# Optimization experiments

Measured on AMD Instinct MI355X. Metric: run time of the kernel, lower is better.

Reference implementation:

```python
import jax, jax.numpy as jnp
import numpy as np

DIM_HEAD = 64
LN_EPS = 1e-6  # flax nn.LayerNorm default


def setup_inputs() -> dict:
    key = jax.random.key(0)
    ks = jax.random.split(key, 5)
    B, N, D, H, Dh = 4, 1024, 768, 12, 64
    x = jax.random.normal(ks[0], (B, N, D), dtype=jnp.float32)
    Wq = jax.random.normal(ks[1], (D, H, Dh), dtype=jnp.float32) * (1.0 / np.sqrt(D))
    Wk = jax.random.normal(ks[2], (D, H, Dh), dtype=jnp.float32) * (1.0 / np.sqrt(D))
    Wv = jax.random.normal(ks[3], (D, H, Dh), dtype=jnp.float32) * (1.0 / np.sqrt(D))
    theta = jax.random.normal(ks[4], (H, H), dtype=jnp.float32) * (1.0 / np.sqrt(H))
    ln_scale = jnp.ones((N,), dtype=jnp.float32)
    ln_bias = jnp.zeros((N,), dtype=jnp.float32)
    return {"x": x, "Wq": Wq, "Wk": Wk, "Wv": Wv, "theta": theta,
            "ln_scale": ln_scale, "ln_bias": ln_bias}


def reference(x, Wq, Wk, Wv, theta, ln_scale, ln_bias):
    # x: [B, N, D]; W*: [D, H, Dh]; theta: [H, H]; ln_*: [N]
    q = jnp.einsum('bnd,dhe->bnhe', x, Wq) / jnp.sqrt(jnp.float32(DIM_HEAD))
    k = jnp.einsum('bnd,dhe->bnhe', x, Wk)
    v = jnp.einsum('bnd,dhe->bnhe', x, Wv)
    # attention scores over key axis: [B, H, N, N]
    attn = jnp.einsum('bqhd,bkhd->bhqk', q, k)
    attn = jax.nn.softmax(attn, axis=-1)
    # cross-head theta mixing: 'h i, b h q k -> b i q k'
    attn = jnp.einsum('hi,bhqk->biqk', theta, attn)
    # LayerNorm over last (key) axis with learnable scale/bias of shape [N]
    mean = jnp.mean(attn, axis=-1, keepdims=True)
    var = jnp.mean(jnp.square(attn - mean), axis=-1, keepdims=True)
    attn = (attn - mean) * jax.lax.rsqrt(var + LN_EPS) * ln_scale + ln_bias
    # note: output indexed by k (as in the original source einsum)
    out = jnp.einsum('bhqk,bqhd->bkhd', attn, v)
    B, N, H, Dh = out.shape
    return out.reshape(B, N, H * Dh)
```

## Files before the change

### kernel.cpp

```cpp
#include <hip/hip_runtime.h>

#define NB    4
#define NSEQ  1024
#define DMODEL 768
#define NH    12
#define DH    64

typedef __bf16 bf16x8 __attribute__((ext_vector_type(8)));
typedef __bf16 bf16x4 __attribute__((ext_vector_type(4)));
typedef float  floatx4 __attribute__((ext_vector_type(4)));
typedef unsigned int u32;

static __device__ __forceinline__ float bf2f(unsigned short u) {
    return __uint_as_float(((unsigned)u) << 16);
}
static __device__ __forceinline__ unsigned short f2bf(float f) {
    unsigned u = __float_as_uint(f);
    u += 0x7FFFu + ((u >> 16) & 1u);
    return (unsigned short)(u >> 16);
}
static __device__ __forceinline__ unsigned short f2bf_hw(float f) {
    __bf16 b = (__bf16)f;
    return *(unsigned short*)&b;
}

static __device__ __forceinline__ void gl_lds16(const void* g, void* l) {
    __builtin_amdgcn_global_load_lds(
        (const __attribute__((address_space(1))) unsigned int*)g,
        (__attribute__((address_space(3))) unsigned int*)l, 16, 0, 0);
}

__global__ __launch_bounds__(256) void cast_x(
    const float* __restrict__ x, unsigned short* __restrict__ xb)
{
    const int g = blockIdx.x * 256 + threadIdx.x;
    const size_t base = (size_t)g * 8;
    float4 a = *(const float4*)(x + base);
    float4 b = *(const float4*)(x + base + 4);
    unsigned short o[8];
    o[0] = f2bf(a.x); o[1] = f2bf(a.y); o[2] = f2bf(a.z); o[3] = f2bf(a.w);
    o[4] = f2bf(b.x); o[5] = f2bf(b.y); o[6] = f2bf(b.z); o[7] = f2bf(b.w);
    *(uint4*)(xb + base) = *(uint4*)o;
}

__global__ __launch_bounds__(256) void tr_w(
    const float* __restrict__ Wq, const float* __restrict__ Wk,
    const float* __restrict__ Wv, unsigned short* __restrict__ Wt)
{
    const int z  = blockIdx.z;
    const float* __restrict__ W = (z == 0) ? Wq : (z == 1) ? Wk : Wv;
    const int c0 = blockIdx.x * 64;
    const int k0 = blockIdx.y * 64;
    const int t  = threadIdx.x;

    __shared__ float ls[64][65];

    const int lr = t >> 2;
    #pragma unroll
    for (int j = 0; j < 4; j++) {
        int col = (t & 3) * 16 + j * 4;
        float4 v = *(const float4*)(W + (size_t)(k0 + lr) * DMODEL + c0 + col);
        ls[lr][col + 0] = v.x; ls[lr][col + 1] = v.y;
        ls[lr][col + 2] = v.z; ls[lr][col + 3] = v.w;
    }
    __syncthreads();
    const int lc = t >> 2;
    #pragma unroll
    for (int j = 0; j < 4; j++) {
        int kb = (t & 3) * 16 + j * 4;
        ushort4 o;
        o.x = f2bf(ls[kb + 0][lc]); o.y = f2bf(ls[kb + 1][lc]);
        o.z = f2bf(ls[kb + 2][lc]); o.w = f2bf(ls[kb + 3][lc]);
        *(ushort4*)(Wt + (size_t)z * DMODEL * DMODEL + (size_t)(c0 + lc) * DMODEL + k0 + kb) = o;
    }
}

__global__ __launch_bounds__(256) void qkv_mfma(
    const unsigned short* __restrict__ xb, const unsigned short* __restrict__ Wt,
    unsigned short* __restrict__ Q, unsigned short* __restrict__ K,
    unsigned short* __restrict__ V)
{
    const int z  = blockIdx.z;
    const int r0 = blockIdx.x * 128;
    const int c0 = blockIdx.y * 128;
    const int t    = threadIdx.x;
    const int wave = t >> 6, lane = t & 63;
    const int m = lane & 15, g = lane >> 4;

    const unsigned short* __restrict__ B = Wt + (size_t)z * DMODEL * DMODEL;

    __shared__ __align__(16) char sm[34816];
    unsigned short (*As)[32] = (unsigned short(*)[32])sm;
    unsigned short (*Bs)[32] = (unsigned short(*)[32])(sm + 8192);
    unsigned short (*Po)[136] = (unsigned short(*)[136])sm;

    const int wm = (wave >> 1) * 64;
    const int wn = (wave & 1) * 64;

    floatx4 acc[4][4] = {};

    const unsigned short* ga0 = xb + (size_t)(r0 + (t >> 2)) * DMODEL + (t & 3) * 8;
    const unsigned short* ga1 = ga0 + (size_t)64 * DMODEL;
    const unsigned short* gb0 = B  + (size_t)(c0 + (t >> 2)) * DMODEL + (t & 3) * 8;
    const unsigned short* gb1 = gb0 + (size_t)64 * DMODEL;
    unsigned short* la0 = (unsigned short*)sm + (size_t)t * 8;
    unsigned short* la1 = la0 + 2048;
    unsigned short* lb0 = (unsigned short*)(sm + 8192) + (size_t)t * 8;
    unsigned short* lb1 = lb0 + 2048;

    for (int kk = 0; kk < DMODEL / 32; kk++) {
        gl_lds16(ga0 + kk * 32, la0);
        gl_lds16(ga1 + kk * 32, la1);
        gl_lds16(gb0 + kk * 32, lb0);
        gl_lds16(gb1 + kk * 32, lb1);
        __syncthreads();

        bf16x8 af[4], bf[4];
        #pragma unroll
        for (int mt = 0; mt < 4; mt++)
            af[mt] = *(const bf16x8*)&As[wm + mt * 16 + m][g * 8];
        #pragma unroll
        for (int nt = 0; nt < 4; nt++)
            bf[nt] = *(const bf16x8*)&Bs[wn + nt * 16 + m][g * 8];
        #pragma unroll
        for (int mt = 0; mt < 4; mt++)
            #pragma unroll
            for (int nt = 0; nt < 4; nt++)
                acc[mt][nt] = __builtin_amdgcn_mfma_f32_16x16x32_bf16(
                    af[mt], bf[nt], acc[mt][nt], 0, 0, 0);
        __syncthreads();
    }

    const float scale = (z == 0) ? 0.125f : 1.0f;
    #pragma unroll
    for (int mt = 0; mt < 4; mt++) {
        #pragma unroll
        for (int nt = 0; nt < 4; nt++) {
            int rloc = wm + mt * 16 + g * 4;
            int cloc = wn + nt * 16 + m;
            #pragma unroll
            for (int r = 0; r < 4; r++)
                Po[rloc + r][cloc] = f2bf(acc[mt][nt][r] * scale);
        }
    }
    __syncthreads();

    #pragma unroll
    for (int i = 0; i < 8; i++) {
        int ci = t + i * 256;
        int row = ci >> 4, off = (ci & 15) * 8;
        uint4 val = *(uint4*)&Po[row][off];
        if (z == 0) {
            *(uint4*)(Q + (size_t)(r0 + row) * DMODEL + c0 + off) = val;
        } else {
            unsigned short* Pp = (z == 1) ? K : V;
            int rr = r0 + row;
            int bb = rr >> 10, n = rr & 1023;
            int cc = c0 + off;
            int h = cc >> 6, d = cc & 63;
            *(uint4*)(Pp + (((size_t)bb * NH + h) * NSEQ + n) * DH + d) = val;
        }
    }
}

__global__ __launch_bounds__(256) void score_gemm(
    const unsigned short* __restrict__ Q, const unsigned short* __restrict__ K,
    unsigned short* __restrict__ P, float* __restrict__ Lpart)
{
    const int bh = blockIdx.z;
    const int b  = bh / NH, h = bh % NH;
    const int q0 = blockIdx.x * 128;
    const int k0 = blockIdx.y * 128;
    const int t    = threadIdx.x;
    const int wave = t >> 6, lane = t & 63;

    __shared__ __align__(16) char sm[36864];
    unsigned short (*Qs)[72] = (unsigned short(*)[72])sm;
    unsigned short (*Ks)[72] = (unsigned short(*)[72])(sm + 18432);
    unsigned short (*Po)[136] = (unsigned short(*)[136])sm;
    float (*rsum)[2] = (float(*)[2])(sm + 34816);

    #pragma unroll
    for (int i = 0; i < 4; i++) {
        int c = t + i * 256;
        int row = c >> 3, off = (c & 7) * 8;
        uint4 qa = *(const uint4*)(Q + ((size_t)(b * NSEQ + q0 + row)) * DMODEL + h * DH + off);
        uint4 ka = *(const uint4*)(K + (((size_t)bh) * NSEQ + (k0 + row)) * DH + off);
        *(uint4*)&Qs[row][off] = qa;
        *(uint4*)&Ks[row][off] = ka;
    }
    __syncthreads();

    const int wq = (wave >> 1) * 64, wk2 = (wave & 1) * 64;
    const int m = lane & 15, g = lane >> 4;

    floatx4 acc[4][4] = {};
    #pragma unroll
    for (int ds = 0; ds < 2; ds++) {
        const int dd = ds * 32 + g * 8;
        bf16x8 af[4], bf[4];
        #pragma unroll
        for (int mt = 0; mt < 4; mt++)
            af[mt] = *(const bf16x8*)&Qs[wq + mt * 16 + m][dd];
        #pragma unroll
        for (int nt = 0; nt < 4; nt++)
            bf[nt] = *(const bf16x8*)&Ks[wk2 + nt * 16 + m][dd];
        #pragma unroll
        for (int mt = 0; mt < 4; mt++)
            #pragma unroll
            for (int nt = 0; nt < 4; nt++)
                acc[mt][nt] = __builtin_amdgcn_mfma_f32_16x16x32_bf16(
                    af[mt], bf[nt], acc[mt][nt], 0, 0, 0);
    }

    __syncthreads();
    float rs[4][4] = {};
    #pragma unroll
    for (int mt = 0; mt < 4; mt++) {
        #pragma unroll
        for (int nt = 0; nt < 4; nt++) {
            int qloc = wq + mt * 16 + g * 4;
            int kloc = wk2 + nt * 16 + m;
            #pragma unroll
            for (int r = 0; r < 4; r++) {
                float e = __expf(acc[mt][nt][r]);
                Po[qloc + r][kloc] = f2bf_hw(e);
                rs[mt][r] += e;
            }
        }
    }
    #pragma unroll
    for (int mt = 0; mt < 4; mt++)
        #pragma unroll
        for (int r = 0; r < 4; r++) {
            float x = rs[mt][r];
            #pragma unroll
            for (int off = 1; off < 16; off <<= 1)
                x += __shfl_xor(x, off, 64);
            rs[mt][r] = x;
        }
    if (m == 0) {
        #pragma unroll
        for (int mt = 0; mt < 4; mt++)
            #pragma unroll
            for (int r = 0; r < 4; r++)
                rsum[wq + mt * 16 + g * 4 + r][wk2 >> 6] = rs[mt][r];
    }
    __syncthreads();

    if (t < 128)
        Lpart[((size_t)bh * 8 + blockIdx.y) * NSEQ + q0 + t] = rsum[t][0] + rsum[t][1];

    #pragma unroll
    for (int i = 0; i < 8; i++) {
        int c = t + i * 256;
        int row = c >> 4, off = (c & 15) * 8;
        *(uint4*)(P + (((size_t)bh * NSEQ) + q0 + row) * NSEQ + k0 + off) =
            *(uint4*)&Po[row][off];
    }
}

__global__ __launch_bounds__(256) void mix_t(
    unsigned short* __restrict__ P, const float* __restrict__ theta,
    const float* __restrict__ Lpart, float* __restrict__ Rbuf)
{
    const int t = threadIdx.x;
    const int wave = t >> 6, lane = t & 63;
    const int q = blockIdx.x, b = blockIdx.y;
    const int k0 = t * 4;

    __shared__ float th_s[144];
    __shared__ float red[4][12];

    unsigned short* Pq = P + ((size_t)b * NH * NSEQ + q) * NSEQ;

    uint2 praw[12];
    #pragma unroll
    for (int h = 0; h < 12; h++)
        praw[h] = *(const uint2*)(Pq + (size_t)h * NSEQ * NSEQ + k0);

    if (t < 144) th_s[t] = theta[t];

    float rl = 0.f;
    if (lane < 12) {
        float s = 0.f;
        #pragma unroll
        for (int kt = 0; kt < 8; kt++)
            s += Lpart[(((size_t)(b * NH + lane)) * 8 + kt) * NSEQ + q];
        rl = 1.0f / s;
    }
    float rlv[12];
    #pragma unroll
    for (int h = 0; h < 12; h++) rlv[h] = __shfl(rl, h, 64);

    __syncthreads();

    float p[12][4];
    #pragma unroll
    for (int h = 0; h < 12; h++) {
        const unsigned short* u = (const unsigned short*)&praw[h];
        p[h][0] = bf2f(u[0]) * rlv[h];
        p[h][1] = bf2f(u[1]) * rlv[h];
        p[h][2] = bf2f(u[2]) * rlv[h];
        p[h][3] = bf2f(u[3]) * rlv[h];
    }

    float rs[12];
    #pragma unroll
    for (int i = 0; i < 12; i++) {
        float s0 = 0.f, s1 = 0.f, s2 = 0.f, s3 = 0.f;
        #pragma unroll
        for (int h = 0; h < 12; h++) {
            float th = th_s[h * 12 + i];
            s0 = fmaf(th, p[h][0], s0); s1 = fmaf(th, p[h][1], s1);
            s2 = fmaf(th, p[h][2], s2); s3 = fmaf(th, p[h][3], s3);
        }
        ushort4 o;
        o.x = f2bf(s0); o.y = f2bf(s1); o.z = f2bf(s2); o.w = f2bf(s3);
        *(ushort4*)(Pq + (size_t)i * NSEQ * NSEQ + k0) = o;
        rs[i] = fmaf(s0, s0, fmaf(s1, s1, fmaf(s2, s2, s3 * s3)));
    }

    #pragma unroll
    for (int i = 0; i < 12; i++) {
        float x = rs[i];
        #pragma unroll
        for (int off = 32; off > 0; off >>= 1)
            x += __shfl_xor(x, off, 64);
        rs[i] = x;
    }
    if (lane < 12) {
        float myrs = 0.f;
        #pragma unroll
        for (int i = 0; i < 12; i++)
            if (lane == i) myrs = rs[i];
        red[wave][lane] = myrs;
    }
    __syncthreads();
    if (t < 12) {
        float sum2 = red[0][t] + red[1][t] + red[2][t] + red[3][t];
        float mean = 0.f;
        #pragma unroll
        for (int h = 0; h < 12; h++) mean += th_s[h * 12 + t];
        mean *= (1.0f / 1024.0f);
        float var = sum2 * (1.0f / 1024.0f) - mean * mean;
        Rbuf[(size_t)(b * NH + t) * NSEQ + q] = rsqrtf(var + 1e-6f);
    }
}

__global__ __launch_bounds__(256) void scale_v(
    const unsigned short* __restrict__ V, const float* __restrict__ Rbuf,
    unsigned short* __restrict__ Vs, float* __restrict__ C1p,
    float* __restrict__ C2p)
{
    const int qh = blockIdx.x;
    const int bi = blockIdx.y;
    const int t  = threadIdx.x;
    const int d4 = (t & 15) * 4;
    const int qg = t >> 4;

    __shared__ float rl_s[256];
    __shared__ float c1l[16][64], c2l[16][64];

    const unsigned short* Vi = V  + (size_t)bi * NSEQ * DH + (size_t)qh * 256 * DH;
    unsigned short*       Vo = Vs + (size_t)bi * NSEQ * DH + (size_t)qh * 256 * DH;
    const float* Rb = Rbuf + (size_t)bi * NSEQ + qh * 256;

    rl_s[t] = Rb[t];
    __syncthreads();

    float s1[4] = {}, s2[4] = {};
    #pragma unroll
    for (int qq = 0; qq < 16; qq++) {
        int q = qg * 16 + qq;
        ushort4 v = *(const ushort4*)(Vi + (size_t)q * DH + d4);
        float r = rl_s[q];
        float f0 = bf2f(v.x), f1 = bf2f(v.y), f2 = bf2f(v.z), f3 = bf2f(v.w);
        float g0 = r * f0, g1 = r * f1, g2 = r * f2, g3 = r * f3;
        ushort4 o;
        o.x = f2bf_hw(g0); o.y = f2bf_hw(g1); o.z = f2bf_hw(g2); o.w = f2bf_hw(g3);
        *(ushort4*)(Vo + (size_t)q * DH + d4) = o;
        s1[0] += g0; s1[1] += g1; s1[2] += g2; s1[3] += g3;
        s2[0] += f0; s2[1] += f1; s2[2] += f2; s2[3] += f3;
    }
    #pragma unroll
    for (int j = 0; j < 4; j++) {
        c1l[qg][d4 + j] = s1[j];
        c2l[qg][d4 + j] = s2[j];
    }
    __syncthreads();
    if (t < 64) {
        float a = 0.f, c = 0.f;
        #pragma unroll
        for (int g2 = 0; g2 < 16; g2++) { a += c1l[g2][t]; c += c2l[g2][t]; }
        C1p[((size_t)bi * 4 + qh) * 64 + t] = a;
        C2p[((size_t)bi * 4 + qh) * 64 + t] = c;
    }
}

__global__ __launch_bounds__(256) void av_mfma(
    const unsigned short* __restrict__ A, const unsigned short* __restrict__ Vs,
    const float* __restrict__ C1p, const float* __restrict__ C2p,
    const float* __restrict__ theta,
    const float* __restrict__ ln_scale, const float* __restrict__ ln_bias,
    float* __restrict__ out)
{
    const int b  = blockIdx.z;
    const int i  = blockIdx.y;
    const int k0 = blockIdx.x * 64;
    const int t  = threadIdx.x;
    const int wave = t >> 6, lane = t & 63;
    const int m = lane & 15, g = lane >> 4;

    __shared__ __align__(16) u32 At[64 * 33];
    __shared__ __align__(16) u32 Vt[64 * 33];

    const int bi = b * NH + i;
    const unsigned short* Ai = A  + (size_t)bi * NSEQ * NSEQ;
    const unsigned short* Vi = Vs + (size_t)bi * NSEQ * DH;

    const int wk = (wave >> 1) * 32;
    const int wd = (wave & 1) * 32;

    floatx4 acc[2][2] = {};

    for (int q0 = 0; q0 < NSEQ; q0 += 64) {
        ushort4 a0[2], a1[2], v0[2], v1[2];
        #pragma unroll
        for (int l = 0; l < 2; l++) {
            int c = t + l * 256;
            int k4 = (c & 15) * 4;
            int qp = c >> 4;
            a0[l] = *(const ushort4*)(Ai + (size_t)(q0 + 2 * qp)     * NSEQ + k0 + k4);
            a1[l] = *(const ushort4*)(Ai + (size_t)(q0 + 2 * qp + 1) * NSEQ + k0 + k4);
            v0[l] = *(const ushort4*)(Vi + (size_t)(q0 + 2 * qp)     * DH + k4);
            v1[l] = *(const ushort4*)(Vi + (size_t)(q0 + 2 * qp + 1) * DH + k4);
        }
        __syncthreads();
        #pragma unroll
        for (int l = 0; l < 2; l++) {
            int c = t + l * 256;
            int k4 = (c & 15) * 4;
            int qp = c >> 4;
            const unsigned short* pa0 = (const unsigned short*)&a0[l];
            const unsigned short* pa1 = (const unsigned short*)&a1[l];
            const unsigned short* pv0 = (const unsigned short*)&v0[l];
            const unsigned short* pv1 = (const unsigned short*)&v1[l];
            #pragma unroll
            for (int j = 0; j < 4; j++) {
                At[(k4 + j) * 33 + qp] = (u32)pa0[j] | ((u32)pa1[j] << 16);
                Vt[(k4 + j) * 33 + qp] = (u32)pv0[j] | ((u32)pv1[j] << 16);
            }
        }
        __syncthreads();

        #pragma unroll
        for (int ks = 0; ks < 2; ks++) {
            const int qo = ks * 16 + g * 4;
            bf16x8 af[2], bf[2];
            #pragma unroll
            for (int mt = 0; mt < 2; mt++) {
                const u32* r = &At[(wk + mt * 16 + m) * 33 + qo];
                uint4 w; w.x = r[0]; w.y = r[1]; w.z = r[2]; w.w = r[3];
                af[mt] = *(bf16x8*)&w;
            }
            #pragma unroll
            for (int nt = 0; nt < 2; nt++) {
                const u32* r = &Vt[(wd + nt * 16 + m) * 33 + qo];
                uint4 w; w.x = r[0]; w.y = r[1]; w.z = r[2]; w.w = r[3];
                bf[nt] = *(bf16x8*)&w;
            }
            #pragma unroll
            for (int mt = 0; mt < 2; mt++)
                #pragma unroll
                for (int nt = 0; nt < 2; nt++)
                    acc[mt][nt] = __builtin_amdgcn_mfma_f32_16x16x32_bf16(
                        af[mt], bf[nt], acc[mt][nt], 0, 0, 0);
        }
    }

    float mean = 0.f;
    #pragma unroll
    for (int h = 0; h < 12; h++) mean += theta[h * 12 + i];
    mean *= (1.0f / 1024.0f);

    #pragma unroll
    for (int mt = 0; mt < 2; mt++) {
        int kb = k0 + wk + mt * 16 + g * 4;
        float4 ls4 = *(const float4*)(ln_scale + kb);
        float4 lb4 = *(const float4*)(ln_bias + kb);
        #pragma unroll
        for (int nt = 0; nt < 2; nt++) {
            int d = wd + nt * 16 + m;
            float C1d = 0.f, C2d = 0.f;
            #pragma unroll
            for (int p4 = 0; p4 < 4; p4++) {
                C1d += C1p[((size_t)bi * 4 + p4) * 64 + d];
                C2d += C2p[((size_t)bi * 4 + p4) * 64 + d];
            }
            #pragma unroll
            for (int r = 0; r < 4; r++) {
                float lns = (&ls4.x)[r], lnb = (&lb4.x)[r];
                float val = lns * (acc[mt][nt][r] - mean * C1d) + lnb * C2d;
                out[((size_t)(b * NSEQ + kb + r)) * DMODEL + i * DH + d] = val;
            }
        }
    }
}

extern "C" void kernel_launch(void* const* d_in, const int* in_sizes, int n_in,
                              void* d_out, int out_size, void* d_ws, size_t ws_size,
                              hipStream_t stream) {
    const float* x     = (const float*)d_in[0];
    const float* Wq    = (const float*)d_in[1];
    const float* Wk    = (const float*)d_in[2];
    const float* Wv    = (const float*)d_in[3];
    const float* theta = (const float*)d_in[4];
    const float* ln_s  = (const float*)d_in[5];
    const float* ln_b  = (const float*)d_in[6];
    float* out = (float*)d_out;

    char* ws = (char*)d_ws;
    const size_t qsz = (size_t)NB * NSEQ * DMODEL * sizeof(unsigned short);
    unsigned short* Q = (unsigned short*)(ws);
    unsigned short* K = (unsigned short*)(ws + qsz);
    unsigned short* V = (unsigned short*)(ws + 2 * qsz);
    unsigned short* P = (unsigned short*)(ws + 3 * qsz);
    unsigned short* xb = P;
    unsigned short* Wt = P + (size_t)NB * NSEQ * DMODEL;

    float* Lpart = out;
    float* Rbuf  = (float*)K;
    unsigned short* Vsb = Q;
    float* C1p = (float*)(ws + qsz + (1u << 20));
    float* C2p = (float*)(ws + qsz + (2u << 20));

    cast_x<<<dim3(NB * NSEQ * DMODEL / 2048), 256, 0, stream>>>(x, xb);
    tr_w<<<dim3(12, 12, 3), 256, 0, stream>>>(Wq, Wk, Wv, Wt);
    qkv_mfma<<<dim3(NB * NSEQ / 128, DMODEL / 128, 3), 256, 0, stream>>>(
        xb, Wt, Q, K, V);
    score_gemm<<<dim3(NSEQ / 128, NSEQ / 128, NB * NH), 256, 0, stream>>>(Q, K, P, Lpart);
    mix_t<<<dim3(NSEQ, NB), 256, 0, stream>>>(P, theta, Lpart, Rbuf);
    scale_v<<<dim3(4, NB * NH), 256, 0, stream>>>(V, Rbuf, Vsb, C1p, C2p);
    av_mfma<<<dim3(NSEQ / 64, NH, NB), 256, 0, stream>>>(
        P, Vsb, C1p, C2p, theta, ln_s, ln_b, out);
}
```

Measured before the change: 213.5 us.

## Recompute scores in mixing kernel instead of materializing exp(P) to HBM

The score kernel now only computes softmax row-sum partials and no longer writes the bf16 exp-score tensor. A new tiled mixing kernel recomputes QK^T for all 12 heads per (q,k) tile, exponentiates, normalizes, applies the theta head mixing and writes the mixed tensor T once. It also emits per-tile partial sums of squares, which a small new reduction kernel turns into the LayerNorm rstd. This removes a full B*H*N*N bf16 write plus read of the exp-score tensor, at the cost of computing the QK^T matmul twice, adding one kernel launch, and giving the mixing kernel a larger shared-memory footprint.

Result: slower. 280.9 us (+31.5%).

```diff
diff --git a/kernel.cpp b/kernel.cpp
--- a/kernel.cpp
+++ b/kernel.cpp
@@ -7,7 +7,6 @@
 #define DH    64
 
 typedef __bf16 bf16x8 __attribute__((ext_vector_type(8)));
-typedef __bf16 bf16x4 __attribute__((ext_vector_type(4)));
 typedef float  floatx4 __attribute__((ext_vector_type(4)));
 typedef unsigned int u32;
 
@@ -163,9 +162,9 @@
     }
 }
 
-__global__ __launch_bounds__(256) void score_gemm(
+__global__ __launch_bounds__(256) void score_l(
     const unsigned short* __restrict__ Q, const unsigned short* __restrict__ K,
-    unsigned short* __restrict__ P, float* __restrict__ Lpart)
+    float* __restrict__ Lpart)
 {
     const int bh = blockIdx.z;
     const int b  = bh / NH, h = bh % NH;
@@ -174,11 +173,9 @@
     const int t    = threadIdx.x;
     const int wave = t >> 6, lane = t & 63;
 
-    __shared__ __align__(16) char sm[36864];
-    unsigned short (*Qs)[72] = (unsigned short(*)[72])sm;
-    unsigned short (*Ks)[72] = (unsigned short(*)[72])(sm + 18432);
-    unsigned short (*Po)[136] = (unsigned short(*)[136])sm;
-    float (*rsum)[2] = (float(*)[2])(sm + 34816);
+    __shared__ __align__(16) unsigned short Qs[128][72];
+    __shared__ __align__(16) unsigned short Ks[128][72];
+    __shared__ float rsum[128][2];
 
     #pragma unroll
     for (int i = 0; i < 4; i++) {
@@ -213,22 +210,14 @@
                     af[mt], bf[nt], acc[mt][nt], 0, 0, 0);
     }
 
-    __syncthreads();
     float rs[4][4] = {};
     #pragma unroll
-    for (int mt = 0; mt < 4; mt++) {
-        #pragma unroll
-        for (int nt = 0; nt < 4; nt++) {
-            int qloc = wq + mt * 16 + g * 4;
-            int kloc = wk2 + nt * 16 + m;
-            #pragma unroll
-            for (int r = 0; r < 4; r++) {
-                float e = __expf(acc[mt][nt][r]);
-                Po[qloc + r][kloc] = f2bf_hw(e);
-                rs[mt][r] += e;
-            }
-        }
-    }
+    for (int mt = 0; mt < 4; mt++)
+        #pragma unroll
+        for (int nt = 0; nt < 4; nt++)
+            #pragma unroll
+            for (int r = 0; r < 4; r++)
+                rs[mt][r] += __expf(acc[mt][nt][r]);
     #pragma unroll
     for (int mt = 0; mt < 4; mt++)
         #pragma unroll
@@ -250,102 +239,145 @@
 
     if (t < 128)
         Lpart[((size_t)bh * 8 + blockIdx.y) * NSEQ + q0 + t] = rsum[t][0] + rsum[t][1];
-
-    #pragma unroll
-    for (int i = 0; i < 8; i++) {
-        int c = t + i * 256;
-        int row = c >> 4, off = (c & 15) * 8;
-        *(uint4*)(P + (((size_t)bh * NSEQ) + q0 + row) * NSEQ + k0 + off) =
-            *(uint4*)&Po[row][off];
-    }
-}
-
-__global__ __launch_bounds__(256) void mix_t(
-    unsigned short* __restrict__ P, const float* __restrict__ theta,
-    const float* __restrict__ Lpart, float* __restrict__ Rbuf)
-{
+}
+
+__global__ __launch_bounds__(256) void mixT(
+    const unsigned short* __restrict__ Q, const unsigned short* __restrict__ K,
+    const float* __restrict__ theta, const float* __restrict__ Lpart,
+    unsigned short* __restrict__ T, float* __restrict__ T2part)
+{
+    const int kt = blockIdx.x;
+    const int qt = blockIdx.y;
+    const int b  = blockIdx.z;
+    const int qg = qt * 64, kg = kt * 32;
     const int t = threadIdx.x;
     const int wave = t >> 6, lane = t & 63;
-    const int q = blockIdx.x, b = blockIdx.y;
-    const int k0 = t * 4;
-
+    const int m = lane & 15, g = lane >> 4;
+
+    __shared__ unsigned short Qs[64][72];
+    __shared__ unsigned short Ks[32][72];
+    __shared__ unsigned short Ph[12][64][36];
+    __shared__ float lq_s[12 * 64];
     __shared__ float th_s[144];
-    __shared__ float red[4][12];
-
-    unsigned short* Pq = P + ((size_t)b * NH * NSEQ + q) * NSEQ;
-
-    uint2 praw[12];
-    #pragma unroll
-    for (int h = 0; h < 12; h++)
-        praw[h] = *(const uint2*)(Pq + (size_t)h * NSEQ * NSEQ + k0);
 
     if (t < 144) th_s[t] = theta[t];
-
-    float rl = 0.f;
-    if (lane < 12) {
-        float s = 0.f;
-        #pragma unroll
-        for (int kt = 0; kt < 8; kt++)
-            s += Lpart[(((size_t)(b * NH + lane)) * 8 + kt) * NSEQ + q];
-        rl = 1.0f / s;
-    }
-    float rlv[12];
-    #pragma unroll
-    for (int h = 0; h < 12; h++) rlv[h] = __shfl(rl, h, 64);
-
-    __syncthreads();
-
-    float p[12][4];
-    #pragma unroll
+    #pragma unroll
+    for (int l = 0; l < 3; l++) {
+        int e = t + l * 256;
+        if (e < 768) {
+            int h = e >> 6, ql = e & 63;
+            float s = 0.f;
+            #pragma unroll
+            for (int k8 = 0; k8 < 8; k8++)
+                s += Lpart[(((size_t)(b * NH + h)) * 8 + k8) * NSEQ + qg + ql];
+            lq_s[e] = 1.0f / s;
+        }
+    }
+
     for (int h = 0; h < 12; h++) {
-        const unsigned short* u = (const unsigned short*)&praw[h];
-        p[h][0] = bf2f(u[0]) * rlv[h];
-        p[h][1] = bf2f(u[1]) * rlv[h];
-        p[h][2] = bf2f(u[2]) * rlv[h];
-        p[h][3] = bf2f(u[3]) * rlv[h];
-    }
-
-    float rs[12];
-    #pragma unroll
-    for (int i = 0; i < 12; i++) {
-        float s0 = 0.f, s1 = 0.f, s2 = 0.f, s3 = 0.f;
+        #pragma unroll
+        for (int l = 0; l < 2; l++) {
+            int c = t + l * 256;
+            int row = c >> 3, off = (c & 7) * 8;
+            *(uint4*)&Qs[row][off] =
+                *(const uint4*)(Q + ((size_t)(b * NSEQ + qg + row)) * DMODEL + h * DH + off);
+        }
+        {
+            int row = t >> 3, off = (t & 7) * 8;
+            *(uint4*)&Ks[row][off] =
+                *(const uint4*)(K + (((size_t)(b * NH + h)) * NSEQ + kg + row) * DH + off);
+        }
+        __syncthreads();
+
+        floatx4 acc[2] = {};
+        #pragma unroll
+        for (int ds = 0; ds < 2; ds++) {
+            int dd = ds * 32 + g * 8;
+            bf16x8 af = *(const bf16x8*)&Qs[wave * 16 + m][dd];
+            #pragma unroll
+            for (int kb = 0; kb < 2; kb++) {
+                bf16x8 bf = *(const bf16x8*)&Ks[kb * 16 + m][dd];
+                acc[kb] = __builtin_amdgcn_mfma_f32_16x16x32_bf16(af, bf, acc[kb], 0, 0, 0);
+            }
+        }
+        #pragma unroll
+        for (int kb = 0; kb < 2; kb++)
+            #pragma unroll
+            for (int r = 0; r < 4; r++)
+                Ph[h][wave * 16 + g * 4 + r][kb * 16 + m] = f2bf_hw(__expf(acc[kb][r]));
+        __syncthreads();
+    }
+
+    #pragma unroll
+    for (int sl = 0; sl < 2; sl++) {
+        int c = t + sl * 256;
+        int q = c >> 3, k4 = (c & 7) * 4;
+
+        float rlv[12];
+        #pragma unroll
+        for (int h = 0; h < 12; h++) rlv[h] = lq_s[h * 64 + q];
+
+        float p[12][4];
         #pragma unroll
         for (int h = 0; h < 12; h++) {
-            float th = th_s[h * 12 + i];
-            s0 = fmaf(th, p[h][0], s0); s1 = fmaf(th, p[h][1], s1);
-            s2 = fmaf(th, p[h][2], s2); s3 = fmaf(th, p[h][3], s3);
-        }
-        ushort4 o;
-        o.x = f2bf(s0); o.y = f2bf(s1); o.z = f2bf(s2); o.w = f2bf(s3);
-        *(ushort4*)(Pq + (size_t)i * NSEQ * NSEQ + k0) = o;
-        rs[i] = fmaf(s0, s0, fmaf(s1, s1, fmaf(s2, s2, s3 * s3)));
-    }
-
-    #pragma unroll
-    for (int i = 0; i < 12; i++) {
-        float x = rs[i];
-        #pragma unroll
-        for (int off = 32; off > 0; off >>= 1)
-            x += __shfl_xor(x, off, 64);
-        rs[i] = x;
-    }
-    if (lane < 12) {
-        float myrs = 0.f;
-        #pragma unroll
-        for (int i = 0; i < 12; i++)
-            if (lane == i) myrs = rs[i];
-        red[wave][lane] = myrs;
-    }
-    __syncthreads();
-    if (t < 12) {
-        float sum2 = red[0][t] + red[1][t] + red[2][t] + red[3][t];
-        float mean = 0.f;
-        #pragma unroll
-        for (int h = 0; h < 12; h++) mean += th_s[h * 12 + t];
-        mean *= (1.0f / 1024.0f);
-        float var = sum2 * (1.0f / 1024.0f) - mean * mean;
-        Rbuf[(size_t)(b * NH + t) * NSEQ + q] = rsqrtf(var + 1e-6f);
-    }
+            const unsigned short* pr = &Ph[h][q][k4];
+            p[h][0] = bf2f(pr[0]) * rlv[h];
+            p[h][1] = bf2f(pr[1]) * rlv[h];
+            p[h][2] = bf2f(pr[2]) * rlv[h];
+            p[h][3] = bf2f(pr[3]) * rlv[h];
+        }
+
+        float rs[12];
+        #pragma unroll
+        for (int i = 0; i < 12; i++) {
+            float s0 = 0.f, s1 = 0.f, s2 = 0.f, s3 = 0.f;
+            #pragma unroll
+            for (int h = 0; h < 12; h++) {
+                float th = th_s[h * 12 + i];
+                s0 = fmaf(th, p[h][0], s0); s1 = fmaf(th, p[h][1], s1);
+                s2 = fmaf(th, p[h][2], s2); s3 = fmaf(th, p[h][3], s3);
+            }
+            ushort4 o;
+            o.x = f2bf(s0); o.y = f2bf(s1); o.z = f2bf(s2); o.w = f2bf(s3);
+            *(ushort4*)(T + (((size_t)(b * NH + i)) * NSEQ + qg + q) * NSEQ + kg + k4) = o;
+            rs[i] = fmaf(s0, s0, fmaf(s1, s1, fmaf(s2, s2, s3 * s3)));
+        }
+
+        #pragma unroll
+        for (int i = 0; i < 12; i++) {
+            float x = rs[i];
+            x += __shfl_xor(x, 1, 64);
+            x += __shfl_xor(x, 2, 64);
+            x += __shfl_xor(x, 4, 64);
+            rs[i] = x;
+        }
+        if ((t & 7) == 0) {
+            #pragma unroll
+            for (int i = 0; i < 12; i++)
+                T2part[(((size_t)(b * NH + i)) * NSEQ + qg + q) * 32 + kt] = rs[i];
+        }
+    }
+}
+
+__global__ __launch_bounds__(256) void rstd_red(
+    const float* __restrict__ T2part, const float* __restrict__ theta,
+    float* __restrict__ Rbuf)
+{
+    const int bi = blockIdx.x;
+    const int i  = bi % NH;
+    const int q  = blockIdx.y * 256 + threadIdx.x;
+
+    float mean = 0.f;
+    #pragma unroll
+    for (int h = 0; h < 12; h++) mean += theta[h * 12 + i];
+    mean *= (1.0f / 1024.0f);
+
+    const float* p = T2part + ((size_t)bi * NSEQ + q) * 32;
+    float s = 0.f;
+    #pragma unroll
+    for (int k = 0; k < 32; k++) s += p[k];
+    float var = s * (1.0f / 1024.0f) - mean * mean;
+    Rbuf[(size_t)bi * NSEQ + q] = rsqrtf(var + 1e-6f);
 }
 
 __global__ __launch_bounds__(256) void scale_v(
@@ -525,23 +557,26 @@
     unsigned short* Q = (unsigned short*)(ws);
     unsigned short* K = (unsigned short*)(ws + qsz);
     unsigned short* V = (unsigned short*)(ws + 2 * qsz);
-    unsigned short* P = (unsigned short*)(ws + 3 * qsz);
-    unsigned short* xb = P;
-    unsigned short* Wt = P + (size_t)NB * NSEQ * DMODEL;
-
-    float* Lpart = out;
-    float* Rbuf  = (float*)K;
+    unsigned short* T = (unsigned short*)(ws + 3 * qsz);
+    unsigned short* xb = T;
+    unsigned short* Wt = T + (size_t)NB * NSEQ * DMODEL;
+
+    float* Lpart  = out;
+    float* T2part = out + (1u << 19);
+    float* Rbuf = (float*)K;
+    float* C1p  = (float*)(ws + qsz + (1u << 20));
+    float* C2p  = (float*)(ws + qsz + (2u << 20));
     unsigned short* Vsb = Q;
-    float* C1p = (float*)(ws + qsz + (1u << 20));
-    float* C2p = (float*)(ws + qsz + (2u << 20));
 
     cast_x<<<dim3(NB * NSEQ * DMODEL / 2048), 256, 0, stream>>>(x, xb);
     tr_w<<<dim3(12, 12, 3), 256, 0, stream>>>(Wq, Wk, Wv, Wt);
     qkv_mfma<<<dim3(NB * NSEQ / 128, DMODEL / 128, 3), 256, 0, stream>>>(
         xb, Wt, Q, K, V);
-    score_gemm<<<dim3(NSEQ / 128, NSEQ / 128, NB * NH), 256, 0, stream>>>(Q, K, P, Lpart);
-    mix_t<<<dim3(NSEQ, NB), 256, 0, stream>>>(P, theta, Lpart, Rbuf);
+    score_l<<<dim3(NSEQ / 128, NSEQ / 128, NB * NH), 256, 0, stream>>>(Q, K, Lpart);
+    mixT<<<dim3(NSEQ / 32, NSEQ / 64, NB), 256, 0, stream>>>(
+        Q, K, theta, Lpart, T, T2part);
+    rstd_red<<<dim3(NB * NH, NSEQ / 256), 256, 0, stream>>>(T2part, theta, Rbuf);
     scale_v<<<dim3(4, NB * NH), 256, 0, stream>>>(V, Rbuf, Vsb, C1p, C2p);
     av_mfma<<<dim3(NSEQ / 64, NH, NB), 256, 0, stream>>>(
-        P, Vsb, C1p, C2p, theta, ln_s, ln_b, out);
-}
+        T, Vsb, C1p, C2p, theta, ln_s, ln_b, out);
+}
```
